# Optimization experiments

Measured on AMD Instinct MI355X. Metric: run time of the kernel, lower is better.

Reference implementation:

```python
import jax, jax.numpy as jnp
import numpy as np

NUM_HEADS = 32
NUM_KV_HEADS = 8
HEAD_DIM = 128
ROPE_THETA = 10000.0


def rotate_half(x):
    half = x.shape[-1] // 2
    return jnp.concatenate([-x[..., half:], x[..., :half]], axis=-1)


def setup_inputs() -> dict:
    key = jax.random.key(0)
    ks = jax.random.split(key, 5)
    b, s, h = 2, 2048, 4096
    kv_dim = NUM_KV_HEADS * HEAD_DIM
    scale = 1.0 / np.sqrt(h)
    return {
        "hidden_states": jax.random.normal(ks[0], (b, s, h), dtype=jnp.float32),
        "position_ids": jnp.broadcast_to(jnp.arange(s, dtype=jnp.int64 if jax.config.jax_enable_x64 else jnp.int32), (b, s)),
        "Wq": jax.random.normal(ks[1], (h, h), dtype=jnp.float32) * scale,
        "Wk": jax.random.normal(ks[2], (h, kv_dim), dtype=jnp.float32) * scale,
        "Wv": jax.random.normal(ks[3], (h, kv_dim), dtype=jnp.float32) * scale,
        "Wo": jax.random.normal(ks[4], (h, h), dtype=jnp.float32) * scale,
    }


def reference(hidden_states, position_ids, Wq, Wk, Wv, Wo):
    b, s, h = hidden_states.shape
    # projections -> [b, heads, s, head_dim]
    q = (hidden_states @ Wq).reshape(b, s, NUM_HEADS, HEAD_DIM).transpose(0, 2, 1, 3)
    k = (hidden_states @ Wk).reshape(b, s, NUM_KV_HEADS, HEAD_DIM).transpose(0, 2, 1, 3)
    v = (hidden_states @ Wv).reshape(b, s, NUM_KV_HEADS, HEAD_DIM).transpose(0, 2, 1, 3)

    # RoPE cache for kv_seq_len = s
    inv_freq = 1.0 / (ROPE_THETA ** (jnp.arange(0, HEAD_DIM, 2, dtype=jnp.float32) / HEAD_DIM))
    freqs = jnp.arange(s, dtype=jnp.float32)[:, None] * inv_freq[None, :]  # [s, hd/2]
    emb = jnp.concatenate([freqs, freqs], axis=-1)                          # [s, hd]
    cos = jnp.cos(emb)[position_ids][:, None, :, :]                         # [b,1,s,hd]
    sin = jnp.sin(emb)[position_ids][:, None, :, :]
    q = q * cos + rotate_half(q) * sin
    k = k * cos + rotate_half(k) * sin

    # GQA expansion (repeat_interleave over head dim)
    groups = NUM_HEADS // NUM_KV_HEADS
    k = jnp.repeat(k, groups, axis=1)
    v = jnp.repeat(v, groups, axis=1)

    scores = jnp.einsum("bhqd,bhkd->bhqk", q, k) / np.sqrt(HEAD_DIM)
    causal = jnp.triu(jnp.full((s, s), -jnp.inf, dtype=scores.dtype), k=1)
    scores = scores + causal
    attn = jax.nn.softmax(scores.astype(jnp.float32), axis=-1).astype(q.dtype)

    out = jnp.einsum("bhqk,bhkd->bhqd", attn, v)
    out = out.transpose(0, 2, 1, 3).reshape(b, s, h)
    return out @ Wo
```

## Files before the change

### kernel.cpp

```cpp
#include <hip/hip_runtime.h>
#include <stdint.h>

typedef unsigned short u16;

#define B_   2
#define S_   2048
#define H_   4096
#define NH   32
#define NKV  8
#define HD   128
#define KVD  (NKV * HD)
#define BS   (B_ * S_)
#define QS   6144
#define KOFF 4096
#define VOFF 5120

typedef __bf16 bf16x8 __attribute__((ext_vector_type(8)));
typedef u16    u16x8  __attribute__((ext_vector_type(8)));
typedef u16    u16x4  __attribute__((ext_vector_type(4)));
typedef float  f32x4  __attribute__((ext_vector_type(4)));

__device__ __forceinline__ bf16x8 as_bf16x8(u16x8 v) { return __builtin_bit_cast(bf16x8, v); }

__device__ __forceinline__ float bf2f(u16 u) {
  union { uint32_t u; float f; } v; v.u = ((uint32_t)u) << 16; return v.f;
}
__device__ __forceinline__ u16 f2bf(float f) {
  return __builtin_bit_cast(u16, (__bf16)f);
}

__device__ __forceinline__ void gload_lds16(const void* g, void* l) {
  __builtin_amdgcn_global_load_lds((const __attribute__((address_space(1))) void*)g,
                                   (__attribute__((address_space(3))) void*)l, 16, 0, 0);
}

__global__ __launch_bounds__(256) void conv_bf16(const float* __restrict__ in,
                                                 u16* __restrict__ out) {
  size_t i = ((size_t)blockIdx.x * 256 + threadIdx.x) * 8;
  float4 a = *(const float4*)(in + i);
  float4 b = *(const float4*)(in + i + 4);
  u16x8 h;
  h[0] = f2bf(a.x); h[1] = f2bf(a.y); h[2] = f2bf(a.z); h[3] = f2bf(a.w);
  h[4] = f2bf(b.x); h[5] = f2bf(b.y); h[6] = f2bf(b.z); h[7] = f2bf(b.w);
  *(u16x8*)(out + i) = h;
}

__global__ __launch_bounds__(256) void conv_transpose_w(const float* __restrict__ in,
                                                        u16* __restrict__ out,
                                                        int ldi, int ldo) {
  __shared__ u16 tile[64][72];
  int r0 = blockIdx.x * 64, c0 = blockIdx.y * 64;
  int t = threadIdx.x;
  {
    int row = t >> 4, col = (t & 15) * 4;
#pragma unroll
    for (int rep = 0; rep < 4; ++rep) {
      int r = row + rep * 16;
      float4 v = *(const float4*)(in + (size_t)(r0 + r) * ldi + c0 + col);
      u16x4 h;
      h[0] = f2bf(v.x); h[1] = f2bf(v.y); h[2] = f2bf(v.z); h[3] = f2bf(v.w);
      *(u16x4*)&tile[r][col] = h;
    }
  }
  __syncthreads();
  {
    int row = t >> 2, c8 = (t & 3) * 8;
#pragma unroll
    for (int it = 0; it < 2; ++it) {
      int rr = c8 + it * 32;
      u16x8 v;
#pragma unroll
      for (int j = 0; j < 8; ++j) v[j] = tile[rr + j][row];
      *(u16x8*)(out + (size_t)(c0 + row) * ldo + r0 + rr) = v;
    }
  }
}

__global__ __launch_bounds__(256) void conv_transpose_w3(const float* __restrict__ Wq,
                                                         const float* __restrict__ Wk,
                                                         const float* __restrict__ Wv,
                                                         u16* __restrict__ Wtq,
                                                         u16* __restrict__ Wtk,
                                                         u16* __restrict__ Wtv) {
  __shared__ u16 tile[64][72];
  int z = blockIdx.z;
  if (z > 0 && blockIdx.y >= 16) return;
  const float* in = (z == 0) ? Wq : (z == 1) ? Wk : Wv;
  u16* out        = (z == 0) ? Wtq : (z == 1) ? Wtk : Wtv;
  int ldi = (z == 0) ? H_ : KVD;
  int r0 = blockIdx.x * 64, c0 = blockIdx.y * 64;
  int t = threadIdx.x;
  {
    int row = t >> 4, col = (t & 15) * 4;
#pragma unroll
    for (int rep = 0; rep < 4; ++rep) {
      int r = row + rep * 16;
      float4 v = *(const float4*)(in + (size_t)(r0 + r) * ldi + c0 + col);
      u16x4 h;
      h[0] = f2bf(v.x); h[1] = f2bf(v.y); h[2] = f2bf(v.z); h[3] = f2bf(v.w);
      *(u16x4*)&tile[r][col] = h;
    }
  }
  __syncthreads();
  {
    int row = t >> 2, c8 = (t & 3) * 8;
#pragma unroll
    for (int it = 0; it < 2; ++it) {
      int rr = c8 + it * 32;
      u16x8 v;
#pragma unroll
      for (int j = 0; j < 8; ++j) v[j] = tile[rr + j][row];
      *(u16x8*)(out + (size_t)(c0 + row) * H_ + r0 + rr) = v;
    }
  }
}

__global__ __launch_bounds__(256) void transpose_v(const u16* __restrict__ QKV,
                                                   u16* __restrict__ Vt) {
  __shared__ u16 tile[64][72];
  int g = blockIdx.z;
  const u16* in = QKV + (size_t)(g >> 3) * ((size_t)S_ * QS) + VOFF + (size_t)(g & 7) * HD;
  u16* out = Vt + (size_t)g * ((size_t)HD * S_);
  int r0 = blockIdx.x * 64, c0 = blockIdx.y * 64;
  int t = threadIdx.x;
  int row = t >> 2, c8 = (t & 3) * 8;
#pragma unroll
  for (int it = 0; it < 2; ++it) {
    int col = c8 + it * 32;
    *(u16x8*)&tile[row][col] = *(const u16x8*)(in + (size_t)(r0 + row) * QS + c0 + col);
  }
  __syncthreads();
#pragma unroll
  for (int it = 0; it < 2; ++it) {
    int rr = c8 + it * 32;
    u16x8 v;
#pragma unroll
    for (int j = 0; j < 8; ++j) v[j] = tile[rr + j][row];
    *(u16x8*)(out + (size_t)(c0 + row) * S_ + r0 + rr) = v;
  }
}

template <bool C_F32>
__global__ __launch_bounds__(256) void gemm_bt_lds(const u16* __restrict__ A,
                                                   const u16* __restrict__ Bt,
                                                   void* __restrict__ Cp,
                                                   int M, int N, int K) {
  __shared__ __align__(16) u16 lsA[128][32];
  __shared__ __align__(16) u16 lsB[128][32];
  int t = threadIdx.x;
  int lane = t & 63;
  int w = t >> 6;
  int wm = (w >> 1) * 64, wn = (w & 1) * 64;
  int bm = blockIdx.x * 128, bn = blockIdx.y * 128;
  int fr = lane & 15, kq = lane >> 4;
  f32x4 acc[4][4] = {};

  int sr = t >> 2, sc = (t & 3) * 8;
  const u16* Ar0 = A + (size_t)(bm + sr) * K + sc;
  const u16* Ar1 = A + (size_t)(bm + sr + 64) * K + sc;
  const u16* Br0 = Bt + (size_t)(bn + sr) * K + sc;
  const u16* Br1 = Bt + (size_t)(bn + sr + 64) * K + sc;
  u16* lA0 = &lsA[sr][sc];
  u16* lA1 = &lsA[sr + 64][sc];
  u16* lB0 = &lsB[sr][sc];
  u16* lB1 = &lsB[sr + 64][sc];

  for (int k0 = 0; k0 < K; k0 += 32) {
    gload_lds16(Ar0 + k0, lA0);
    gload_lds16(Ar1 + k0, lA1);
    gload_lds16(Br0 + k0, lB0);
    gload_lds16(Br1 + k0, lB1);
    __syncthreads();
    bf16x8 af[4], bfr[4];
#pragma unroll
    for (int i = 0; i < 4; ++i) af[i] = as_bf16x8(*(const u16x8*)&lsA[wm + i * 16 + fr][kq * 8]);
#pragma unroll
    for (int j = 0; j < 4; ++j) bfr[j] = as_bf16x8(*(const u16x8*)&lsB[wn + j * 16 + fr][kq * 8]);
#pragma unroll
    for (int i = 0; i < 4; ++i)
#pragma unroll
      for (int j = 0; j < 4; ++j)
        acc[i][j] = __builtin_amdgcn_mfma_f32_16x16x32_bf16(af[i], bfr[j], acc[i][j], 0, 0, 0);
    __syncthreads();
  }
#pragma unroll
  for (int i = 0; i < 4; ++i)
#pragma unroll
    for (int j = 0; j < 4; ++j)
#pragma unroll
      for (int r = 0; r < 4; ++r) {
        int row = bm + wm + i * 16 + kq * 4 + r;
        int col = bn + wn + j * 16 + fr;
        if (C_F32) ((float*)Cp)[(size_t)row * N + col] = acc[i][j][r];
        else       ((u16*)Cp)[(size_t)row * N + col] = f2bf(acc[i][j][r]);
      }
}

__global__ __launch_bounds__(256) void gemm_qkv(const u16* __restrict__ A,
                                                const u16* __restrict__ Wtq,
                                                const u16* __restrict__ Wtk,
                                                const u16* __restrict__ Wtv,
                                                u16* __restrict__ C) {
  const int K = H_;
  __shared__ __align__(16) u16 lsA[128][32];
  __shared__ __align__(16) u16 lsB[128][32];
  int t = threadIdx.x;
  int lane = t & 63;
  int w = t >> 6;
  int wm = (w >> 1) * 64, wn = (w & 1) * 64;
  int bm = blockIdx.x * 128;
  int by = blockIdx.y;
  const u16* Bt; int bnl;
  if (by < 32)      { Bt = Wtq; bnl = by * 128; }
  else if (by < 40) { Bt = Wtk; bnl = (by - 32) * 128; }
  else              { Bt = Wtv; bnl = (by - 40) * 128; }
  int bn = by * 128;
  int fr = lane & 15, kq = lane >> 4;
  f32x4 acc[4][4] = {};

  int sr = t >> 2, sc = (t & 3) * 8;
  const u16* Ar0 = A + (size_t)(bm + sr) * K + sc;
  const u16* Ar1 = Ar0 + (size_t)64 * K;
  const u16* Br0 = Bt + (size_t)(bnl + sr) * K + sc;
  const u16* Br1 = Br0 + (size_t)64 * K;
  u16* lA0 = &lsA[sr][sc];
  u16* lA1 = &lsA[sr + 64][sc];
  u16* lB0 = &lsB[sr][sc];
  u16* lB1 = &lsB[sr + 64][sc];

  for (int k0 = 0; k0 < K; k0 += 32) {
    gload_lds16(Ar0 + k0, lA0);
    gload_lds16(Ar1 + k0, lA1);
    gload_lds16(Br0 + k0, lB0);
    gload_lds16(Br1 + k0, lB1);
    __syncthreads();
    bf16x8 af[4], bfr[4];
#pragma unroll
    for (int i = 0; i < 4; ++i) af[i] = as_bf16x8(*(const u16x8*)&lsA[wm + i * 16 + fr][kq * 8]);
#pragma unroll
    for (int j = 0; j < 4; ++j) bfr[j] = as_bf16x8(*(const u16x8*)&lsB[wn + j * 16 + fr][kq * 8]);
#pragma unroll
    for (int i = 0; i < 4; ++i)
#pragma unroll
      for (int j = 0; j < 4; ++j)
        acc[i][j] = __builtin_amdgcn_mfma_f32_16x16x32_bf16(af[i], bfr[j], acc[i][j], 0, 0, 0);
    __syncthreads();
  }
#pragma unroll
  for (int i = 0; i < 4; ++i)
#pragma unroll
    for (int j = 0; j < 4; ++j)
#pragma unroll
      for (int r = 0; r < 4; ++r) {
        int row = bm + wm + i * 16 + kq * 4 + r;
        int col = bn + wn + j * 16 + fr;
        C[(size_t)row * QS + col] = f2bf(acc[i][j][r]);
      }
}

__global__ __launch_bounds__(256) void rope_kernel(u16* __restrict__ QKV) {
  int idx = blockIdx.x * 256 + threadIdx.x;
  int j = idx & 63;
  int rem = idx >> 6;
  int hh = rem % 40;
  int tok = rem / 40;
  float p = (float)(tok % S_);
  float freq = __expf((float)j * (-9.210340371976184f / 64.0f));
  float sn, cs;
  __sincosf(p * freq, &sn, &cs);
  u16* base = QKV + (size_t)tok * QS + (size_t)hh * HD;
  float x1 = bf2f(base[j]), x2 = bf2f(base[j + 64]);
  base[j]      = f2bf(x1 * cs - x2 * sn);
  base[j + 64] = f2bf(x2 * cs + x1 * sn);
}

__global__ __launch_bounds__(512) void flash_attn(const u16* __restrict__ QKV,
                                                  const u16* __restrict__ Vt,
                                                  u16* __restrict__ O) {
  __shared__ __align__(16) u16 Ks[64 * 128];
  __shared__ __align__(16) u16 Vs[64 * 128];
  __shared__ u16 Plds[8][16][72];
  int qt = (gridDim.x - 1) - blockIdx.x;
  int kvh = blockIdx.y, b = blockIdx.z;
  int t = threadIdx.x, lane = t & 63, w = t >> 6;
  int h = kvh * 4 + (w & 3);
  int u = w >> 2;
  int fr = lane & 15, kq = lane >> 4;
  int q0 = qt * 32 + u * 16;

  const u16* qbase = QKV + (size_t)(b * S_ + q0 + fr) * QS + (size_t)h * HD;
  bf16x8 qf[4];
#pragma unroll
  for (int kk = 0; kk < 4; ++kk) qf[kk] = as_bf16x8(*(const u16x8*)(qbase + kk * 32 + kq * 8));

  f32x4 o[8] = {};
  float mrow[4] = {-1e30f, -1e30f, -1e30f, -1e30f};
  float lrow[4] = {0.f, 0.f, 0.f, 0.f};

  const u16* kbase = QKV + (size_t)(b * S_) * QS + KOFF + (size_t)kvh * HD;
  const u16* vbase = Vt + (size_t)(b * NKV + kvh) * ((size_t)HD * S_);
  const float scale = 0.08838834764831845f;

  int krow0 = t >> 4, kc = t & 15;
  int vrow0 = t >> 3, vc = t & 7;

  int niter = (qt * 32 + 31) / 64 + 1;

  u16x8 kreg[2], vreg[2];
#pragma unroll
  for (int ps = 0; ps < 2; ++ps) {
    int row = krow0 + ps * 32;
    kreg[ps] = *(const u16x8*)(kbase + (size_t)row * QS + kc * 8);
    int vrow = vrow0 + ps * 64;
    vreg[ps] = *(const u16x8*)(vbase + (size_t)vrow * S_ + vc * 8);
  }

  for (int kt = 0; kt < niter; ++kt) {
    int k0 = kt * 64;
    if (kt) __syncthreads();
#pragma unroll
    for (int ps = 0; ps < 2; ++ps) {
      int row = krow0 + ps * 32;
      *(u16x8*)&Ks[row * 128 + ((kc ^ row) & 15) * 8] = kreg[ps];
      int vrow = vrow0 + ps * 64;
      int vrho = vrow >> 1;
      int vcw  = (vrow & 1) * 8 + vc;
      *(u16x8*)&Vs[vrho * 128 + ((vcw ^ vrho) & 15) * 8] = vreg[ps];
    }
    __syncthreads();
    if (kt + 1 < niter) {
      int k1 = k0 + 64;
#pragma unroll
      for (int ps = 0; ps < 2; ++ps) {
        int row = krow0 + ps * 32;
        kreg[ps] = *(const u16x8*)(kbase + (size_t)(k1 + row) * QS + kc * 8);
        int vrow = vrow0 + ps * 64;
        vreg[ps] = *(const u16x8*)(vbase + (size_t)vrow * S_ + k1 + vc * 8);
      }
    }

    f32x4 s[4] = {};
    __builtin_amdgcn_s_setprio(1);
#pragma unroll
    for (int kk = 0; kk < 4; ++kk) {
#pragma unroll
      for (int j = 0; j < 4; ++j) {
        bf16x8 kf = as_bf16x8(*(const u16x8*)&Ks[(j * 16 + fr) * 128 + (((kk * 4 + kq) ^ fr) & 15) * 8]);
        s[j] = __builtin_amdgcn_mfma_f32_16x16x32_bf16(qf[kk], kf, s[j], 0, 0, 0);
      }
    }
    __builtin_amdgcn_s_setprio(0);
    float mt[4] = {-1e30f, -1e30f, -1e30f, -1e30f};
#pragma unroll
    for (int j = 0; j < 4; ++j) {
      int kv = k0 + j * 16 + fr;
#pragma unroll
      for (int r = 0; r < 4; ++r) {
        int qr = q0 + kq * 4 + r;
        float sv = (kv <= qr) ? s[j][r] * scale : -1e30f;
        s[j][r] = sv;
        mt[r] = fmaxf(mt[r], sv);
      }
    }
#pragma unroll
    for (int off = 1; off < 16; off <<= 1)
#pragma unroll
      for (int r = 0; r < 4; ++r) mt[r] = fmaxf(mt[r], __shfl_xor(mt[r], off, 64));

    float alpha[4], lt[4];
#pragma unroll
    for (int r = 0; r < 4; ++r) {
      float mn = fmaxf(mrow[r], mt[r]);
      alpha[r] = __expf(mrow[r] - mn);
      mrow[r] = mn;
      lt[r] = 0.f;
    }
#pragma unroll
    for (int j = 0; j < 4; ++j)
#pragma unroll
      for (int r = 0; r < 4; ++r) {
        float p = __expf(s[j][r] - mrow[r]);
        s[j][r] = p;
        lt[r] += p;
      }
#pragma unroll
    for (int off = 1; off < 16; off <<= 1)
#pragma unroll
      for (int r = 0; r < 4; ++r) lt[r] += __shfl_xor(lt[r], off, 64);
#pragma unroll
    for (int r = 0; r < 4; ++r) lrow[r] = lrow[r] * alpha[r] + lt[r];
#pragma unroll
    for (int tt = 0; tt < 8; ++tt)
#pragma unroll
      for (int r = 0; r < 4; ++r) o[tt][r] *= alpha[r];

#pragma unroll
    for (int j = 0; j < 4; ++j)
#pragma unroll
      for (int r = 0; r < 4; ++r)
        Plds[w][kq * 4 + r][j * 16 + fr] = f2bf(s[j][r]);

#pragma unroll
    for (int st = 0; st < 2; ++st) {
      bf16x8 pf = as_bf16x8(*(const u16x8*)&Plds[w][fr][st * 32 + kq * 8]);
      __builtin_amdgcn_s_setprio(1);
#pragma unroll
      for (int tt = 0; tt < 8; ++tt) {
        int d = tt * 16 + fr;
        int rho = tt * 8 + (fr >> 1);
        int c = (fr & 1) * 8 + st * 4 + kq;
        bf16x8 vv = as_bf16x8(*(const u16x8*)&Vs[rho * 128 + ((c ^ rho) & 15) * 8]);
        o[tt] = __builtin_amdgcn_mfma_f32_16x16x32_bf16(pf, vv, o[tt], 0, 0, 0);
      }
      __builtin_amdgcn_s_setprio(0);
    }
  }

  float inv[4];
#pragma unroll
  for (int r = 0; r < 4; ++r) inv[r] = 1.0f / lrow[r];
  u16* obase = O + (size_t)(b * S_ + q0) * H_ + (size_t)h * HD;
#pragma unroll
  for (int tt = 0; tt < 8; ++tt)
#pragma unroll
    for (int r = 0; r < 4; ++r)
      obase[(size_t)(kq * 4 + r) * H_ + tt * 16 + fr] = f2bf(o[tt][r] * inv[r]);
}

extern "C" void kernel_launch(void* const* d_in, const int* in_sizes, int n_in,
                              void* d_out, int out_size, void* d_ws, size_t ws_size,
                              hipStream_t stream) {
  const float* X  = (const float*)d_in[0];
  const float* Wq = (const float*)d_in[2];
  const float* Wk = (const float*)d_in[3];
  const float* Wv = (const float*)d_in[4];
  const float* Wo = (const float*)d_in[5];
  float* out = (float*)d_out;

  char* ws = (char*)d_ws;
  u16* Wtk = (u16*)ws;
  u16* Vt  = (u16*)(ws + 8ull  * 1024 * 1024);
  u16* Xb  = (u16*)(ws + 16ull * 1024 * 1024);
  u16* Ob  = (u16*)(ws + 16ull * 1024 * 1024);
  u16* Wtq = (u16*)(ws + 48ull * 1024 * 1024);
  u16* QKV = (u16*)d_out;
  u16* Wtv = (u16*)((char*)d_out + 48ull * 1024 * 1024);

  dim3 blk(256);
  dim3 blk8(512);

  conv_bf16<<<dim3((size_t)BS * H_ / 8 / 256), blk, 0, stream>>>(X, Xb);

  conv_transpose_w3<<<dim3(64, 64, 3), blk, 0, stream>>>(Wq, Wk, Wv, Wtq, Wtk, Wtv);

  gemm_qkv<<<dim3(32, 48), blk, 0, stream>>>(Xb, Wtq, Wtk, Wtv, QKV);

  rope_kernel<<<dim3((BS * 40 * 64) / 256), blk, 0, stream>>>(QKV);
  transpose_v<<<dim3(S_ / 64, HD / 64, B_ * NKV), blk, 0, stream>>>(QKV, Vt);
  flash_attn<<<dim3(S_ / 32, NKV, B_), blk8, 0, stream>>>(QKV, Vt, Ob);
  conv_transpose_w<<<dim3(64, 64), blk, 0, stream>>>(Wo, Wtq, H_, H_);
  gemm_bt_lds<true><<<dim3(32, 32), blk, 0, stream>>>(Ob, Wtq, out, BS, H_, H_);
}
```

Baseline: 942.0 us.

## Use exp2 softmax with lazy rescale, skip masking off-diagonal, pad V tile

Folds the attention scale into an exp2 base conversion, computed with the raw v_exp_f32 instruction. Causal masking now runs only on tiles that touch the diagonal. The online-softmax rescale of the O accumulators and l is skipped whenever no row's max grows by more than a threshold, which cuts VALU work per KV tile. The V shared-memory tile moves from an XOR-swizzled layout to a padded [128][72] layout with simpler indexing. The lazy rescale lets the row max lag behind, so exponentials can reach larger values; the threshold keeps them inside fp32 range, but this changes the numerics.

```diff
diff --git a/kernel.cpp b/kernel.cpp
--- a/kernel.cpp
+++ b/kernel.cpp
@@ -27,6 +27,11 @@
 }
 __device__ __forceinline__ u16 f2bf(float f) {
   return __builtin_bit_cast(u16, (__bf16)f);
+}
+__device__ __forceinline__ float fast_exp2(float x) {
+  float r;
+  asm("v_exp_f32 %0, %1" : "=v"(r) : "v"(x));
+  return r;
 }
 
 __device__ __forceinline__ void gload_lds16(const void* g, void* l) {
@@ -278,7 +283,7 @@
                                                   const u16* __restrict__ Vt,
                                                   u16* __restrict__ O) {
   __shared__ __align__(16) u16 Ks[64 * 128];
-  __shared__ __align__(16) u16 Vs[64 * 128];
+  __shared__ __align__(16) u16 Vs[128][72];
   __shared__ u16 Plds[8][16][72];
   int qt = (gridDim.x - 1) - blockIdx.x;
   int kvh = blockIdx.y, b = blockIdx.z;
@@ -299,7 +304,8 @@
 
   const u16* kbase = QKV + (size_t)(b * S_) * QS + KOFF + (size_t)kvh * HD;
   const u16* vbase = Vt + (size_t)(b * NKV + kvh) * ((size_t)HD * S_);
-  const float scale = 0.08838834764831845f;
+  const float SC2 = 0.12751745f;
+  const float THR = 90.5f;
 
   int krow0 = t >> 4, kc = t & 15;
   int vrow0 = t >> 3, vc = t & 7;
@@ -323,9 +329,7 @@
       int row = krow0 + ps * 32;
       *(u16x8*)&Ks[row * 128 + ((kc ^ row) & 15) * 8] = kreg[ps];
       int vrow = vrow0 + ps * 64;
-      int vrho = vrow >> 1;
-      int vcw  = (vrow & 1) * 8 + vc;
-      *(u16x8*)&Vs[vrho * 128 + ((vcw ^ vrho) & 15) * 8] = vreg[ps];
+      *(u16x8*)&Vs[vrow][vc * 8] = vreg[ps];
     }
     __syncthreads();
     if (kt + 1 < niter) {
@@ -350,36 +354,51 @@
       }
     }
     __builtin_amdgcn_s_setprio(0);
+
     float mt[4] = {-1e30f, -1e30f, -1e30f, -1e30f};
-#pragma unroll
-    for (int j = 0; j < 4; ++j) {
-      int kv = k0 + j * 16 + fr;
+    if (k0 + 63 > q0) {
+#pragma unroll
+      for (int j = 0; j < 4; ++j) {
+        int kv = k0 + j * 16 + fr;
+#pragma unroll
+        for (int r = 0; r < 4; ++r) {
+          int qr = q0 + kq * 4 + r;
+          float sv = (kv <= qr) ? s[j][r] : -1e30f;
+          s[j][r] = sv;
+          mt[r] = fmaxf(mt[r], sv);
+        }
+      }
+    } else {
+#pragma unroll
+      for (int j = 0; j < 4; ++j)
+#pragma unroll
+        for (int r = 0; r < 4; ++r) mt[r] = fmaxf(mt[r], s[j][r]);
+    }
+#pragma unroll
+    for (int off = 1; off < 16; off <<= 1)
+#pragma unroll
+      for (int r = 0; r < 4; ++r) mt[r] = fmaxf(mt[r], __shfl_xor(mt[r], off, 64));
+
+    float g = fmaxf(fmaxf(mt[0] - mrow[0], mt[1] - mrow[1]),
+                    fmaxf(mt[2] - mrow[2], mt[3] - mrow[3]));
+    if (!__all(g <= THR)) {
 #pragma unroll
       for (int r = 0; r < 4; ++r) {
-        int qr = q0 + kq * 4 + r;
-        float sv = (kv <= qr) ? s[j][r] * scale : -1e30f;
-        s[j][r] = sv;
-        mt[r] = fmaxf(mt[r], sv);
-      }
-    }
-#pragma unroll
-    for (int off = 1; off < 16; off <<= 1)
-#pragma unroll
-      for (int r = 0; r < 4; ++r) mt[r] = fmaxf(mt[r], __shfl_xor(mt[r], off, 64));
-
-    float alpha[4], lt[4];
-#pragma unroll
-    for (int r = 0; r < 4; ++r) {
-      float mn = fmaxf(mrow[r], mt[r]);
-      alpha[r] = __expf(mrow[r] - mn);
-      mrow[r] = mn;
-      lt[r] = 0.f;
-    }
+        float mn = fmaxf(mrow[r], mt[r]);
+        float a = fast_exp2((mrow[r] - mn) * SC2);
+        mrow[r] = mn;
+        lrow[r] *= a;
+#pragma unroll
+        for (int tt = 0; tt < 8; ++tt) o[tt][r] *= a;
+      }
+    }
+
+    float lt[4] = {0.f, 0.f, 0.f, 0.f};
 #pragma unroll
     for (int j = 0; j < 4; ++j)
 #pragma unroll
       for (int r = 0; r < 4; ++r) {
-        float p = __expf(s[j][r] - mrow[r]);
+        float p = fast_exp2((s[j][r] - mrow[r]) * SC2);
         s[j][r] = p;
         lt[r] += p;
       }
@@ -388,11 +407,7 @@
 #pragma unroll
       for (int r = 0; r < 4; ++r) lt[r] += __shfl_xor(lt[r], off, 64);
 #pragma unroll
-    for (int r = 0; r < 4; ++r) lrow[r] = lrow[r] * alpha[r] + lt[r];
-#pragma unroll
-    for (int tt = 0; tt < 8; ++tt)
-#pragma unroll
-      for (int r = 0; r < 4; ++r) o[tt][r] *= alpha[r];
+    for (int r = 0; r < 4; ++r) lrow[r] += lt[r];
 
 #pragma unroll
     for (int j = 0; j < 4; ++j)
@@ -406,10 +421,7 @@
       __builtin_amdgcn_s_setprio(1);
 #pragma unroll
       for (int tt = 0; tt < 8; ++tt) {
-        int d = tt * 16 + fr;
-        int rho = tt * 8 + (fr >> 1);
-        int c = (fr & 1) * 8 + st * 4 + kq;
-        bf16x8 vv = as_bf16x8(*(const u16x8*)&Vs[rho * 128 + ((c ^ rho) & 15) * 8]);
+        bf16x8 vv = as_bf16x8(*(const u16x8*)&Vs[tt * 16 + fr][st * 32 + kq * 8]);
         o[tt] = __builtin_amdgcn_mfma_f32_16x16x32_bf16(pf, vv, o[tt], 0, 0, 0);
       }
       __builtin_amdgcn_s_setprio(0);
```

After: 922.2 us. 2.1% less time.
